# Performance work log

Measured on AMD Instinct MI355X. Metric: run time of the kernel, lower is better.

## Reference

```python
import jax, jax.numpy as jnp
import numpy as np

GROUP_SIZE = 128
N_BITS = 4
QMAX = 2 ** N_BITS - 1
NUM_EXPERTS = 8
HIDDEN = 2048
INTER = 768
NUM_ROT = 4
T_TOKENS = 4096
TOP_K = 2


def _make_pairs(rng, n_rot, in_feat):
    # intra-group permutation per rotation (valid disjoint Givens pairs)
    n_groups = in_feat // GROUP_SIZE
    return np.stack([
        np.concatenate([rng.permutation(GROUP_SIZE) for _ in range(n_groups)])
        for _ in range(n_rot)
    ]).astype(np.int32)


def _round_ste(x):
    return x + jax.lax.stop_gradient(jnp.round(x) - x)


def _rotate(W, pairs, angles):
    # W: [N, in_feat]; pairs: [R, in_feat] intra-group perm; angles: [R, in_feat//2]
    in_feat = W.shape[1]
    base = (jnp.arange(in_feat) // GROUP_SIZE) * GROUP_SIZE
    for r in range(pairs.shape[0]):
        abs_idx = base + pairs[r]
        i_idx = abs_idx[0::2]
        j_idx = abs_idx[1::2]
        c = jnp.cos(angles[r])
        s = jnp.sin(angles[r])
        wi = W[:, i_idx]
        wj = W[:, j_idx]
        W = W.at[:, i_idx].set(c * wi - s * wj).at[:, j_idx].set(s * wi + c * wj)
    return W


def _fake_quant(W):
    # groupwise asymmetric min-max fake quantization with STE rounding
    shape = W.shape
    wg = W.reshape(-1, GROUP_SIZE)
    wmax = wg.max(axis=-1, keepdims=True)
    wmin = wg.min(axis=-1, keepdims=True)
    scale = jnp.clip(wmax - wmin, 1e-5, None) / QMAX
    zero = jnp.round(-wmin / scale)
    q = jnp.clip(_round_ste(wg / scale) + zero, 0.0, float(QMAX))
    return ((q - zero) * scale).reshape(shape)


def _pseudo_quantize(W3, pairs, angles, ch_scales):
    # scale -> rotate -> fake-quant -> inverse rotate (reversed order, -angles) -> unscale
    E, O, In = W3.shape
    W = W3.reshape(-1, In) * ch_scales
    W = _rotate(W, pairs, angles)
    W = _fake_quant(W)
    W = _rotate(W, pairs[::-1], -angles[::-1])
    return (W / ch_scales).reshape(E, O, In)


def setup_inputs() -> dict:
    key = jax.random.key(0)
    ks = jax.random.split(key, 8)
    rng = np.random.default_rng(0)
    hidden_states = jax.random.normal(ks[0], (T_TOKENS, HIDDEN), jnp.float32)
    top_k_index = jax.random.randint(ks[1], (T_TOKENS, TOP_K), 0, NUM_EXPERTS, jnp.int32)
    logits = jax.random.normal(ks[2], (T_TOKENS, TOP_K), jnp.float32)
    top_k_weights = jax.nn.softmax(logits, axis=-1)
    gate_up_weight = jax.random.normal(ks[3], (NUM_EXPERTS, 2 * INTER, HIDDEN), jnp.float32) * 0.02
    down_weight = jax.random.normal(ks[4], (NUM_EXPERTS, HIDDEN, INTER), jnp.float32) * 0.02
    gate_up_pairs = jnp.asarray(_make_pairs(rng, NUM_ROT, HIDDEN))
    down_pairs = jnp.asarray(_make_pairs(rng, NUM_ROT, INTER))
    gate_up_angles = jax.random.normal(ks[5], (NUM_ROT, HIDDEN // 2), jnp.float32) * 0.1
    down_angles = jax.random.normal(ks[6], (NUM_ROT, INTER // 2), jnp.float32) * 0.1
    k7, k8 = jax.random.split(ks[7])
    gate_up_channel_scales = jax.random.uniform(k7, (1, HIDDEN), jnp.float32, 0.5, 1.5)
    down_channel_scales = jax.random.uniform(k8, (1, INTER), jnp.float32, 0.5, 1.5)
    return {
        "hidden_states": hidden_states,
        "top_k_index": top_k_index,
        "top_k_weights": top_k_weights,
        "gate_up_weight": gate_up_weight,
        "down_weight": down_weight,
        "gate_up_pairs": gate_up_pairs,
        "gate_up_angles": gate_up_angles,
        "down_pairs": down_pairs,
        "down_angles": down_angles,
        "gate_up_channel_scales": gate_up_channel_scales,
        "down_channel_scales": down_channel_scales,
    }


def reference(hidden_states, top_k_index, top_k_weights, gate_up_weight, down_weight,
              gate_up_pairs, gate_up_angles, down_pairs, down_angles,
              gate_up_channel_scales, down_channel_scales):
    # dequantize expert weights
    gup = _pseudo_quantize(gate_up_weight, gate_up_pairs, gate_up_angles, gate_up_channel_scales)  # [E,2I,H]
    dwn = _pseudo_quantize(down_weight, down_pairs, down_angles, down_channel_scales)              # [E,H,I]
    T = hidden_states.shape[0]
    E = gup.shape[0]
    # dense dispatch: all experts for all tokens (E small), combined by routing weights
    h = jnp.einsum('th,eoh->teo', hidden_states, gup)          # [T,E,2I]
    gate, up = jnp.split(h, 2, axis=-1)
    inter = jax.nn.silu(gate) * up                              # [T,E,I]
    y = jnp.einsum('tei,ehi->teh', inter, dwn)                  # [T,E,H]
    combine = jnp.zeros((T, E), hidden_states.dtype)
    combine = combine.at[jnp.arange(T)[:, None], top_k_index].add(top_k_weights)
    return jnp.einsum('teh,te->th', y, combine)
```

## Files before the change

kernel.cpp:

```cpp
#include <hip/hip_runtime.h>

#define T_TOKENS 4096
#define HIDDEN   2048
#define INTERM   768
#define NE       8
#define NPAIR    8192
#define NROT     4
#define MAXT     72

typedef __bf16 bf16x8 __attribute__((ext_vector_type(8)));
typedef float  f32x4  __attribute__((ext_vector_type(4)));

__device__ __forceinline__ unsigned short f2bf(float f) {
  unsigned u = __float_as_uint(f);
  u += 0x7fffu + ((u >> 16) & 1u);
  return (unsigned short)(u >> 16);
}

__device__ __forceinline__ void async16(const void* g, void* l) {
  __builtin_amdgcn_global_load_lds((const __attribute__((address_space(1))) void*)g,
                                   (__attribute__((address_space(3))) void*)l, 16, 0, 0);
}

__global__ void k_hist(const int* __restrict__ idx, int* __restrict__ cnt) {
  const int t = blockIdx.x * 256 + threadIdx.x;
  if (t < NPAIR) atomicAdd(&cnt[idx[t]], 1);
}

__global__ void k_scan(const int* __restrict__ cnt, int* __restrict__ off,
                       int* __restrict__ cur, int* __restrict__ tmap) {
  if (threadIdx.x == 0) {
    int a = 0, tt = 0;
    for (int e = 0; e < NE; ++e) {
      off[e] = a; cur[e] = 0;
      const int c = cnt[e];
      for (int m = 0; m < c; m += 128) tmap[tt++] = (e << 16) | (m >> 7);
      a += c;
    }
    for (; tt < MAXT; ++tt) tmap[tt] = -1;
  }
}

__global__ void k_scatter(const int* __restrict__ idx, const float* __restrict__ wts,
                          const int* __restrict__ off, int* __restrict__ cur,
                          int* __restrict__ pt, float* __restrict__ pw) {
  const int t = blockIdx.x * 256 + threadIdx.x;
  if (t < NPAIR) {
    const int e = idx[t];
    const int pos = off[e] + atomicAdd(&cur[e], 1);
    pt[pos] = t >> 1;
    pw[pos] = wts[t];
  }
}

__global__ void k_cvt(const float4* __restrict__ X, ushort4* __restrict__ out) {
  const int t = blockIdx.x * 256 + threadIdx.x;
  const float4 v = X[t];
  ushort4 o;
  o.x = f2bf(v.x); o.y = f2bf(v.y); o.z = f2bf(v.z); o.w = f2bf(v.w);
  out[t] = o;
}

__global__ void k_tbl(const int* __restrict__ gp, const float* __restrict__ ga,
                      const int* __restrict__ dp, const float* __restrict__ da,
                      const float* __restrict__ gch, const float* __restrict__ dch,
                      float4* __restrict__ tg, float4* __restrict__ td,
                      float* __restrict__ grch, float* __restrict__ drch) {
  const int t = blockIdx.x * 256 + threadIdx.x;
  if (t < NROT * (HIDDEN / 2)) {
    const int r = t >> 10, s = t & 1023;
    const int grp = s >> 6;
    const int i = gp[r * HIDDEN + 2 * s], j = gp[r * HIDDEN + 2 * s + 1];
    const float a = ga[r * (HIDDEN / 2) + s];
    const float c = cosf(a), sn = sinf(a);
    tg[(grp * NROT + r) * 128 + i] = make_float4(c, -sn, __int_as_float(j), 0.f);
    tg[(grp * NROT + r) * 128 + j] = make_float4(c,  sn, __int_as_float(i), 0.f);
  }
  if (t < NROT * (INTERM / 2)) {
    const int r = t / (INTERM / 2), s = t - r * (INTERM / 2);
    const int grp = s >> 6;
    const int i = dp[r * INTERM + 2 * s], j = dp[r * INTERM + 2 * s + 1];
    const float a = da[r * (INTERM / 2) + s];
    const float c = cosf(a), sn = sinf(a);
    td[(grp * NROT + r) * 128 + i] = make_float4(c, -sn, __int_as_float(j), 0.f);
    td[(grp * NROT + r) * 128 + j] = make_float4(c,  sn, __int_as_float(i), 0.f);
  }
  if (t < HIDDEN) grch[t] = 1.0f / gch[t];
  if (t < INTERM) drch[t] = 1.0f / dch[t];
}

__global__ __launch_bounds__(256) void k_quant(
    const float* __restrict__ W, const float4* __restrict__ tbl,
    const float* __restrict__ ch, const float* __restrict__ rch,
    unsigned short* __restrict__ out, int In, int G) {
  __shared__ float4 tl[NROT * 128];
  const int wv = threadIdx.x >> 6, l = threadIdx.x & 63;
  const int g = blockIdx.x % G;
  const int rowblk = blockIdx.x / G;
  const int row0 = rowblk * 16 + wv * 4;
  const int colbase = g << 7;
  tl[threadIdx.x]       = tbl[(size_t)g * NROT * 128 + threadIdx.x];
  tl[256 + threadIdx.x] = tbl[(size_t)g * NROT * 128 + 256 + threadIdx.x];
  __syncthreads();
  const float c0 = ch[colbase + l], c1 = ch[colbase + 64 + l];
  const float i0 = rch[colbase + l], i1 = rch[colbase + 64 + l];
  float v0[4], v1[4];
#pragma unroll
  for (int q = 0; q < 4; ++q) {
#pragma clang fp contract(off)
    const float* Wr = W + (size_t)(row0 + q) * In + colbase;
    v0[q] = Wr[l] * c0;
    v1[q] = Wr[64 + l] * c1;
  }
#pragma unroll
  for (int r = 0; r < NROT; ++r) {
    const float4 e0 = tl[r * 128 + l];
    const float4 e1 = tl[r * 128 + 64 + l];
    const int p0 = __float_as_int(e0.z), p1 = __float_as_int(e1.z);
    const int a0 = (p0 & 63) << 2, a1 = (p1 & 63) << 2;
#pragma unroll
    for (int q = 0; q < 4; ++q) {
      const int x0 = __float_as_int(v0[q]), x1 = __float_as_int(v1[q]);
      const float lo0 = __int_as_float(__builtin_amdgcn_ds_bpermute(a0, x0));
      const float hi0 = __int_as_float(__builtin_amdgcn_ds_bpermute(a0, x1));
      const float lo1 = __int_as_float(__builtin_amdgcn_ds_bpermute(a1, x0));
      const float hi1 = __int_as_float(__builtin_amdgcn_ds_bpermute(a1, x1));
      const float op0 = (p0 & 64) ? hi0 : lo0;
      const float op1 = (p1 & 64) ? hi1 : lo1;
      {
#pragma clang fp contract(off)
        v0[q] = e0.x * v0[q] + e0.y * op0;
        v1[q] = e1.x * v1[q] + e1.y * op1;
      }
    }
  }
#pragma unroll
  for (int q = 0; q < 4; ++q) {
    float mn = fminf(v0[q], v1[q]), mx = fmaxf(v0[q], v1[q]);
#pragma unroll
    for (int o = 32; o > 0; o >>= 1) {
      mn = fminf(mn, __shfl_xor(mn, o));
      mx = fmaxf(mx, __shfl_xor(mx, o));
    }
    {
#pragma clang fp contract(off)
      const float scale = fmaxf(mx - mn, 1e-5f) / 15.0f;
      const float zero = rintf(-mn / scale);
      const float q0 = fminf(fmaxf(rintf(v0[q] / scale) + zero, 0.0f), 15.0f);
      const float q1 = fminf(fmaxf(rintf(v1[q] / scale) + zero, 0.0f), 15.0f);
      v0[q] = (q0 - zero) * scale;
      v1[q] = (q1 - zero) * scale;
    }
  }
#pragma unroll
  for (int r = NROT - 1; r >= 0; --r) {
    const float4 e0 = tl[r * 128 + l];
    const float4 e1 = tl[r * 128 + 64 + l];
    const int p0 = __float_as_int(e0.z), p1 = __float_as_int(e1.z);
    const int a0 = (p0 & 63) << 2, a1 = (p1 & 63) << 2;
#pragma unroll
    for (int q = 0; q < 4; ++q) {
      const int x0 = __float_as_int(v0[q]), x1 = __float_as_int(v1[q]);
      const float lo0 = __int_as_float(__builtin_amdgcn_ds_bpermute(a0, x0));
      const float hi0 = __int_as_float(__builtin_amdgcn_ds_bpermute(a0, x1));
      const float lo1 = __int_as_float(__builtin_amdgcn_ds_bpermute(a1, x0));
      const float hi1 = __int_as_float(__builtin_amdgcn_ds_bpermute(a1, x1));
      const float op0 = (p0 & 64) ? hi0 : lo0;
      const float op1 = (p1 & 64) ? hi1 : lo1;
      {
#pragma clang fp contract(off)
        v0[q] = e0.x * v0[q] - e0.y * op0;
        v1[q] = e1.x * v1[q] - e1.y * op1;
      }
    }
  }
#pragma unroll
  for (int q = 0; q < 4; ++q) {
    unsigned short* Or = out + (size_t)(row0 + q) * In + colbase;
    Or[l]      = f2bf(v0[q] * i0);
    Or[64 + l] = f2bf(v1[q] * i1);
  }
}

template <int MODE>
__launch_bounds__(256, 4)
__global__ void k_gemm(const unsigned short* __restrict__ A,
                       const unsigned short* __restrict__ Bw,
                       float* __restrict__ C,
                       const int* __restrict__ pt,
                       const int* __restrict__ off,
                       const int* __restrict__ cnt,
                       const int* __restrict__ tmap) {
  constexpr int K = MODE ? INTERM : HIDDEN;
  constexpr int N = MODE ? HIDDEN : 2 * INTERM;
  const int tm = tmap[blockIdx.y];
  if (tm < 0) return;
  const int e = tm >> 16;
  const int m0 = (tm & 0xffff) << 7;
  const int count = cnt[e];
  const int seg = off[e];
  const int n0 = blockIdx.x * 128;
  const unsigned short* Be = Bw + (size_t)e * N * K;

  __shared__ unsigned short As[2][128 * 32];
  __shared__ unsigned short Bs[2][128 * 32];

  const int tid = threadIdx.x;
  const int w = tid >> 6;
  const int l = tid & 63;
  const int r0 = w * 16 + (l >> 2);
  const int r1 = r0 + 64;
  const int kco = (l & 3) * 8;

  int p0 = m0 + r0; if (p0 > count - 1) p0 = count - 1;
  int p1 = m0 + r1; if (p1 > count - 1) p1 = count - 1;
  size_t arow0, arow1;
  if (MODE == 0) { arow0 = pt[seg + p0]; arow1 = pt[seg + p1]; }
  else           { arow0 = (size_t)(seg + p0); arow1 = (size_t)(seg + p1); }
  const unsigned short* pa0 = A + arow0 * K + kco;
  const unsigned short* pa1 = A + arow1 * K + kco;
  const unsigned short* pb0 = Be + (size_t)(n0 + r0) * K + kco;
  const unsigned short* pb1 = Be + (size_t)(n0 + r1) * K + kco;

  const int ko = (l >> 4) * 8;
  const int mrow = (w & 1) * 64 + (l & 15);
  const int nrow = (w >> 1) * 64 + (l & 15);

  f32x4 acc[4][4];
#pragma unroll
  for (int i = 0; i < 4; ++i)
#pragma unroll
    for (int j = 0; j < 4; ++j) acc[i][j] = (f32x4)0.0f;

  {
    async16(pa0, &As[0][w * 512]);
    async16(pa1, &As[0][(w + 4) * 512]);
    async16(pb0, &Bs[0][w * 512]);
    async16(pb1, &Bs[0][(w + 4) * 512]);
  }
  int buf = 0;
  for (int k0 = 0; k0 < K; k0 += 32, buf ^= 1) {
    __syncthreads();
    bf16x8 af[4], bfr[4];
#pragma unroll
    for (int i = 0; i < 4; ++i)
      af[i] = *(const bf16x8*)&As[buf][(mrow + i * 16) * 32 + ko];
#pragma unroll
    for (int j = 0; j < 4; ++j)
      bfr[j] = *(const bf16x8*)&Bs[buf][(nrow + j * 16) * 32 + ko];
    if (k0 + 32 < K) {
      const int kn = k0 + 32;
      async16(pa0 + kn, &As[buf ^ 1][w * 512]);
      async16(pa1 + kn, &As[buf ^ 1][(w + 4) * 512]);
      async16(pb0 + kn, &Bs[buf ^ 1][w * 512]);
      async16(pb1 + kn, &Bs[buf ^ 1][(w + 4) * 512]);
    }
#pragma unroll
    for (int i = 0; i < 4; ++i)
#pragma unroll
      for (int j = 0; j < 4; ++j)
        acc[i][j] = __builtin_amdgcn_mfma_f32_16x16x32_bf16(af[i], bfr[j], acc[i][j], 0, 0, 0);
  }

  const int mb = (w & 1) * 64 + (l >> 4) * 4;
  const int nb = n0 + (w >> 1) * 64 + (l & 15);
#pragma unroll
  for (int i = 0; i < 4; ++i) {
#pragma unroll
    for (int j = 0; j < 4; ++j) {
#pragma unroll
      for (int r = 0; r < 4; ++r) {
        const int mm = m0 + mb + i * 16 + r;
        if (mm < count) {
          const int nn = nb + j * 16;
          if (MODE == 0) {
            C[(size_t)(seg + mm) * N + nn] = acc[i][j][r];
          } else {
            atomicAdd(&C[(size_t)pt[seg + mm] * N + nn], acc[i][j][r]);
          }
        }
      }
    }
  }
}

__global__ void k_silu(const float* __restrict__ h, const float* __restrict__ pw,
                       ushort4* __restrict__ inter) {
  const int t = blockIdx.x * 256 + threadIdx.x;
  const int p = t / 192;
  const int i4 = (t - p * 192) * 4;
  const float4 g = *(const float4*)&h[(size_t)p * 1536 + i4];
  const float4 u = *(const float4*)&h[(size_t)p * 1536 + 768 + i4];
  const float wgt = pw[p];
  ushort4 o;
  o.x = f2bf(g.x / (1.0f + expf(-g.x)) * u.x * wgt);
  o.y = f2bf(g.y / (1.0f + expf(-g.y)) * u.y * wgt);
  o.z = f2bf(g.z / (1.0f + expf(-g.z)) * u.z * wgt);
  o.w = f2bf(g.w / (1.0f + expf(-g.w)) * u.w * wgt);
  inter[(size_t)p * 192 + (i4 >> 2)] = o;
}

extern "C" void kernel_launch(void* const* d_in, const int* in_sizes, int n_in,
                              void* d_out, int out_size, void* d_ws, size_t ws_size,
                              hipStream_t stream) {
  const float* hs  = (const float*)d_in[0];
  const int*   tki = (const int*)d_in[1];
  const float* tkw = (const float*)d_in[2];
  const float* guw = (const float*)d_in[3];
  const float* dww = (const float*)d_in[4];
  const int*   gupr= (const int*)d_in[5];
  const float* gua = (const float*)d_in[6];
  const int*   dwp = (const int*)d_in[7];
  const float* dwa = (const float*)d_in[8];
  const float* gus = (const float*)d_in[9];
  const float* dwsc= (const float*)d_in[10];
  float* out = (float*)d_out;
  char* ws = (char*)d_ws;

  unsigned short* gup_bf = (unsigned short*)(ws + 0);
  unsigned short* dwn_bf = (unsigned short*)(ws + 50331648);
  unsigned short* x_bf   = (unsigned short*)(ws + 75497472);
  float*          hbuf   = (float*)(ws + 92274688);
  unsigned short* interb = (unsigned short*)(ws + 142606336);
  int*            pt     = (int*)(ws + 155189248);
  float*          pw     = (float*)(ws + 155222016);
  int*            cnt    = (int*)(ws + 155254784);
  int*            off    = cnt + 8;
  int*            cur    = cnt + 16;
  int*            tmap   = cnt + 24;
  float4*         tg     = (float4*)(ws + 155258880);
  float4*         td     = (float4*)(ws + 155389952);
  float*          grch   = (float*)(ws + 155439104);
  float*          drch   = (float*)(ws + 155447296);

  (void)hipMemsetAsync(d_out, 0, (size_t)T_TOKENS * HIDDEN * sizeof(float), stream);
  (void)hipMemsetAsync(cnt, 0, 32, stream);

  k_hist<<<32, 256, 0, stream>>>(tki, cnt);
  k_scan<<<1, 64, 0, stream>>>(cnt, off, cur, tmap);
  k_scatter<<<32, 256, 0, stream>>>(tki, tkw, off, cur, pt, pw);
  k_cvt<<<8192, 256, 0, stream>>>((const float4*)hs, (ushort4*)x_bf);
  k_tbl<<<16, 256, 0, stream>>>(gupr, gua, dwp, dwa, gus, dwsc, tg, td, grch, drch);
  k_quant<<<12288, 256, 0, stream>>>(guw, tg, gus, grch, gup_bf, HIDDEN, 16);
  k_quant<<<6144, 256, 0, stream>>>(dww, td, dwsc, drch, dwn_bf, INTERM, 6);
  k_gemm<0><<<dim3(12, MAXT), 256, 0, stream>>>(x_bf, gup_bf, hbuf, pt, off, cnt, tmap);
  k_silu<<<6144, 256, 0, stream>>>(hbuf, pw, (ushort4*)interb);
  k_gemm<1><<<dim3(16, MAXT), 256, 0, stream>>>(interb, dwn_bf, out, pt, off, cnt, tmap);
}
```

Baseline: 624.5 us.

## Move inverse rotation and unscale from weights onto activations

The weight dequant no longer applies the inverse Givens rotation and channel unscale. It stores the quantized weights still in the rotated domain. Because the rotation is orthogonal, the same rotation plus the 1/scale is applied to the activations instead: the hidden states in a new conversion kernel, and the SiLU output in a fused silu+rotate kernel. This halves the rotation work in the large weight-quant kernels but adds rotation work on the token activations, and it changes rounding order relative to the reference.

```diff
diff --git a/kernel.cpp b/kernel.cpp
--- a/kernel.cpp
+++ b/kernel.cpp
@@ -51,14 +51,6 @@
     pt[pos] = t >> 1;
     pw[pos] = wts[t];
   }
-}
-
-__global__ void k_cvt(const float4* __restrict__ X, ushort4* __restrict__ out) {
-  const int t = blockIdx.x * 256 + threadIdx.x;
-  const float4 v = X[t];
-  ushort4 o;
-  o.x = f2bf(v.x); o.y = f2bf(v.y); o.z = f2bf(v.z); o.w = f2bf(v.w);
-  out[t] = o;
 }
 
 __global__ void k_tbl(const int* __restrict__ gp, const float* __restrict__ ga,
@@ -89,10 +81,33 @@
   if (t < INTERM) drch[t] = 1.0f / dch[t];
 }
 
+#define FWD_ROT(tl, v0, v1)                                                     \
+  _Pragma("unroll")                                                             \
+  for (int r = 0; r < NROT; ++r) {                                              \
+    const float4 e0 = tl[r * 128 + l];                                          \
+    const float4 e1 = tl[r * 128 + 64 + l];                                     \
+    const int p0 = __float_as_int(e0.z), p1 = __float_as_int(e1.z);             \
+    const int a0 = (p0 & 63) << 2, a1 = (p1 & 63) << 2;                         \
+    _Pragma("unroll")                                                           \
+    for (int q = 0; q < 4; ++q) {                                               \
+      const int x0 = __float_as_int(v0[q]), x1 = __float_as_int(v1[q]);         \
+      const float lo0 = __int_as_float(__builtin_amdgcn_ds_bpermute(a0, x0));   \
+      const float hi0 = __int_as_float(__builtin_amdgcn_ds_bpermute(a0, x1));   \
+      const float lo1 = __int_as_float(__builtin_amdgcn_ds_bpermute(a1, x0));   \
+      const float hi1 = __int_as_float(__builtin_amdgcn_ds_bpermute(a1, x1));   \
+      const float op0 = (p0 & 64) ? hi0 : lo0;                                  \
+      const float op1 = (p1 & 64) ? hi1 : lo1;                                  \
+      {                                                                         \
+        _Pragma("clang fp contract(off)")                                       \
+        v0[q] = e0.x * v0[q] + e0.y * op0;                                      \
+        v1[q] = e1.x * v1[q] + e1.y * op1;                                      \
+      }                                                                         \
+    }                                                                           \
+  }
+
 __global__ __launch_bounds__(256) void k_quant(
     const float* __restrict__ W, const float4* __restrict__ tbl,
-    const float* __restrict__ ch, const float* __restrict__ rch,
-    unsigned short* __restrict__ out, int In, int G) {
+    const float* __restrict__ ch, unsigned short* __restrict__ out, int In, int G) {
   __shared__ float4 tl[NROT * 128];
   const int wv = threadIdx.x >> 6, l = threadIdx.x & 63;
   const int g = blockIdx.x % G;
@@ -103,7 +118,6 @@
   tl[256 + threadIdx.x] = tbl[(size_t)g * NROT * 128 + 256 + threadIdx.x];
   __syncthreads();
   const float c0 = ch[colbase + l], c1 = ch[colbase + 64 + l];
-  const float i0 = rch[colbase + l], i1 = rch[colbase + 64 + l];
   float v0[4], v1[4];
 #pragma unroll
   for (int q = 0; q < 4; ++q) {
@@ -112,28 +126,7 @@
     v0[q] = Wr[l] * c0;
     v1[q] = Wr[64 + l] * c1;
   }
-#pragma unroll
-  for (int r = 0; r < NROT; ++r) {
-    const float4 e0 = tl[r * 128 + l];
-    const float4 e1 = tl[r * 128 + 64 + l];
-    const int p0 = __float_as_int(e0.z), p1 = __float_as_int(e1.z);
-    const int a0 = (p0 & 63) << 2, a1 = (p1 & 63) << 2;
-#pragma unroll
-    for (int q = 0; q < 4; ++q) {
-      const int x0 = __float_as_int(v0[q]), x1 = __float_as_int(v1[q]);
-      const float lo0 = __int_as_float(__builtin_amdgcn_ds_bpermute(a0, x0));
-      const float hi0 = __int_as_float(__builtin_amdgcn_ds_bpermute(a0, x1));
-      const float lo1 = __int_as_float(__builtin_amdgcn_ds_bpermute(a1, x0));
-      const float hi1 = __int_as_float(__builtin_amdgcn_ds_bpermute(a1, x1));
-      const float op0 = (p0 & 64) ? hi0 : lo0;
-      const float op1 = (p1 & 64) ? hi1 : lo1;
-      {
-#pragma clang fp contract(off)
-        v0[q] = e0.x * v0[q] + e0.y * op0;
-        v1[q] = e1.x * v1[q] + e1.y * op1;
-      }
-    }
-  }
+  FWD_ROT(tl, v0, v1)
 #pragma unroll
   for (int q = 0; q < 4; ++q) {
     float mn = fminf(v0[q], v1[q]), mx = fmaxf(v0[q], v1[q]);
@@ -153,32 +146,73 @@
     }
   }
 #pragma unroll
-  for (int r = NROT - 1; r >= 0; --r) {
-    const float4 e0 = tl[r * 128 + l];
-    const float4 e1 = tl[r * 128 + 64 + l];
-    const int p0 = __float_as_int(e0.z), p1 = __float_as_int(e1.z);
-    const int a0 = (p0 & 63) << 2, a1 = (p1 & 63) << 2;
-#pragma unroll
-    for (int q = 0; q < 4; ++q) {
-      const int x0 = __float_as_int(v0[q]), x1 = __float_as_int(v1[q]);
-      const float lo0 = __int_as_float(__builtin_amdgcn_ds_bpermute(a0, x0));
-      const float hi0 = __int_as_float(__builtin_amdgcn_ds_bpermute(a0, x1));
-      const float lo1 = __int_as_float(__builtin_amdgcn_ds_bpermute(a1, x0));
-      const float hi1 = __int_as_float(__builtin_amdgcn_ds_bpermute(a1, x1));
-      const float op0 = (p0 & 64) ? hi0 : lo0;
-      const float op1 = (p1 & 64) ? hi1 : lo1;
-      {
-#pragma clang fp contract(off)
-        v0[q] = e0.x * v0[q] - e0.y * op0;
-        v1[q] = e1.x * v1[q] - e1.y * op1;
-      }
-    }
-  }
-#pragma unroll
   for (int q = 0; q < 4; ++q) {
     unsigned short* Or = out + (size_t)(row0 + q) * In + colbase;
-    Or[l]      = f2bf(v0[q] * i0);
-    Or[64 + l] = f2bf(v1[q] * i1);
+    Or[l]      = f2bf(v0[q]);
+    Or[64 + l] = f2bf(v1[q]);
+  }
+}
+
+__global__ __launch_bounds__(256) void k_rotx(
+    const float* __restrict__ X, const float* __restrict__ rch,
+    const float4* __restrict__ tbl, unsigned short* __restrict__ out) {
+  __shared__ float4 tl[NROT * 128];
+  const int wv = threadIdx.x >> 6, l = threadIdx.x & 63;
+  const int g = blockIdx.x % 16;
+  const int rowblk = blockIdx.x / 16;
+  const int row0 = rowblk * 16 + wv * 4;
+  const int colbase = g << 7;
+  tl[threadIdx.x]       = tbl[(size_t)g * NROT * 128 + threadIdx.x];
+  tl[256 + threadIdx.x] = tbl[(size_t)g * NROT * 128 + 256 + threadIdx.x];
+  __syncthreads();
+  const float i0 = rch[colbase + l], i1 = rch[colbase + 64 + l];
+  float v0[4], v1[4];
+#pragma unroll
+  for (int q = 0; q < 4; ++q) {
+    const float* Xr = X + (size_t)(row0 + q) * HIDDEN + colbase;
+    v0[q] = Xr[l] * i0;
+    v1[q] = Xr[64 + l] * i1;
+  }
+  FWD_ROT(tl, v0, v1)
+#pragma unroll
+  for (int q = 0; q < 4; ++q) {
+    unsigned short* Or = out + (size_t)(row0 + q) * HIDDEN + colbase;
+    Or[l]      = f2bf(v0[q]);
+    Or[64 + l] = f2bf(v1[q]);
+  }
+}
+
+__global__ __launch_bounds__(256) void k_silu2(
+    const float* __restrict__ h, const float* __restrict__ pw,
+    const float* __restrict__ rch, const float4* __restrict__ tbl,
+    unsigned short* __restrict__ out) {
+  __shared__ float4 tl[NROT * 128];
+  const int wv = threadIdx.x >> 6, l = threadIdx.x & 63;
+  const int g = blockIdx.x % 6;
+  const int rowblk = blockIdx.x / 6;
+  const int row0 = rowblk * 16 + wv * 4;
+  const int colbase = g << 7;
+  tl[threadIdx.x]       = tbl[(size_t)g * NROT * 128 + threadIdx.x];
+  tl[256 + threadIdx.x] = tbl[(size_t)g * NROT * 128 + 256 + threadIdx.x];
+  __syncthreads();
+  const float i0 = rch[colbase + l], i1 = rch[colbase + 64 + l];
+  float v0[4], v1[4];
+#pragma unroll
+  for (int q = 0; q < 4; ++q) {
+    const int row = row0 + q;
+    const float wgt = pw[row];
+    const float* hr = h + (size_t)row * 1536 + colbase;
+    const float g0 = hr[l], g1 = hr[64 + l];
+    const float u0 = hr[768 + l], u1 = hr[768 + 64 + l];
+    v0[q] = g0 / (1.0f + expf(-g0)) * u0 * wgt * i0;
+    v1[q] = g1 / (1.0f + expf(-g1)) * u1 * wgt * i1;
+  }
+  FWD_ROT(tl, v0, v1)
+#pragma unroll
+  for (int q = 0; q < 4; ++q) {
+    unsigned short* Or = out + (size_t)(row0 + q) * INTERM + colbase;
+    Or[l]      = f2bf(v0[q]);
+    Or[64 + l] = f2bf(v1[q]);
   }
 }
 
@@ -284,22 +318,6 @@
   }
 }
 
-__global__ void k_silu(const float* __restrict__ h, const float* __restrict__ pw,
-                       ushort4* __restrict__ inter) {
-  const int t = blockIdx.x * 256 + threadIdx.x;
-  const int p = t / 192;
-  const int i4 = (t - p * 192) * 4;
-  const float4 g = *(const float4*)&h[(size_t)p * 1536 + i4];
-  const float4 u = *(const float4*)&h[(size_t)p * 1536 + 768 + i4];
-  const float wgt = pw[p];
-  ushort4 o;
-  o.x = f2bf(g.x / (1.0f + expf(-g.x)) * u.x * wgt);
-  o.y = f2bf(g.y / (1.0f + expf(-g.y)) * u.y * wgt);
-  o.z = f2bf(g.z / (1.0f + expf(-g.z)) * u.z * wgt);
-  o.w = f2bf(g.w / (1.0f + expf(-g.w)) * u.w * wgt);
-  inter[(size_t)p * 192 + (i4 >> 2)] = o;
-}
-
 extern "C" void kernel_launch(void* const* d_in, const int* in_sizes, int n_in,
                               void* d_out, int out_size, void* d_ws, size_t ws_size,
                               hipStream_t stream) {
@@ -339,11 +357,11 @@
   k_hist<<<32, 256, 0, stream>>>(tki, cnt);
   k_scan<<<1, 64, 0, stream>>>(cnt, off, cur, tmap);
   k_scatter<<<32, 256, 0, stream>>>(tki, tkw, off, cur, pt, pw);
-  k_cvt<<<8192, 256, 0, stream>>>((const float4*)hs, (ushort4*)x_bf);
   k_tbl<<<16, 256, 0, stream>>>(gupr, gua, dwp, dwa, gus, dwsc, tg, td, grch, drch);
-  k_quant<<<12288, 256, 0, stream>>>(guw, tg, gus, grch, gup_bf, HIDDEN, 16);
-  k_quant<<<6144, 256, 0, stream>>>(dww, td, dwsc, drch, dwn_bf, INTERM, 6);
+  k_rotx<<<4096, 256, 0, stream>>>(hs, grch, tg, x_bf);
+  k_quant<<<12288, 256, 0, stream>>>(guw, tg, gus, gup_bf, HIDDEN, 16);
+  k_quant<<<6144, 256, 0, stream>>>(dww, td, dwsc, dwn_bf, INTERM, 6);
   k_gemm<0><<<dim3(12, MAXT), 256, 0, stream>>>(x_bf, gup_bf, hbuf, pt, off, cnt, tmap);
-  k_silu<<<6144, 256, 0, stream>>>(hbuf, pw, (ushort4*)interb);
+  k_silu2<<<3072, 256, 0, stream>>>(hbuf, pw, drch, td, interb);
   k_gemm<1><<<dim3(16, MAXT), 256, 0, stream>>>(interb, dwn_bf, out, pt, off, cnt, tmap);
 }
```

Measured after the change: 581.5 us. 1.07x faster.
